# Kernel optimization log

Hardware: AMD Instinct MI355X
Metric: run time of the kernel (lower is better)

Reference implementation:

```python
import jax, jax.numpy as jnp
import numpy as np

B, T, C = 4, 2048, 1024
H = 16
D = C // H  # head_dim = 64

def setup_inputs() -> dict:
    key = jax.random.key(0)
    ks = jax.random.split(key, 5)
    s = 0.02
    return {
        "x": jax.random.normal(ks[0], (B, T, C), dtype=jnp.float32),
        "qkv_w": jax.random.normal(ks[1], (3 * C, C), dtype=jnp.float32) * s,
        "qkv_b": jax.random.normal(ks[2], (3 * C,), dtype=jnp.float32) * s,
        "proj_w": jax.random.normal(ks[3], (C, C), dtype=jnp.float32) * s,
        "proj_b": jax.random.normal(ks[4], (C,), dtype=jnp.float32) * s,
    }

def reference(x, qkv_w, qkv_b, proj_w, proj_b):
    Bx, Tx, Cx = x.shape
    # QKV projection (torch Linear: x @ W^T + b)
    qkv = x @ qkv_w.T + qkv_b                       # [B,T,3C]
    qkv = qkv.reshape(Bx, Tx, 3, H, D)
    qkv = jnp.transpose(qkv, (2, 0, 3, 1, 4))       # [3,B,H,T,D]
    q, k, v = qkv[0], qkv[1], qkv[2]
    scale = D ** -0.5
    attn = jnp.einsum("bhqd,bhkd->bhqk", q, k) * scale  # [B,H,T,T]
    causal = jnp.tril(jnp.ones((Tx, Tx), dtype=bool))
    attn = jnp.where(causal, attn, -jnp.inf)
    attn = jax.nn.softmax(attn, axis=-1)
    # dropout is identity in eval mode
    out = jnp.einsum("bhqk,bhkd->bhqd", attn, v)    # [B,H,T,D]
    out = jnp.transpose(out, (0, 2, 1, 3)).reshape(Bx, Tx, Cx)
    return out @ proj_w.T + proj_b
```

## Files before the change

### kernel.cpp

```cpp
#include <hip/hip_runtime.h>
#include <cstdint>
#include <cstddef>

#define B_ 4
#define T_ 2048
#define C_ 1024
#define H_ 16
#define D_ 64

typedef __bf16 bf16;
typedef __bf16 bf16x4 __attribute__((ext_vector_type(4)));
typedef __bf16 bf16x8 __attribute__((ext_vector_type(8)));
typedef float f32x4 __attribute__((ext_vector_type(4)));
typedef float f32x16 __attribute__((ext_vector_type(16)));
typedef unsigned int u32x4v __attribute__((ext_vector_type(4)));

typedef __attribute__((address_space(1))) void gvoid;
typedef __attribute__((address_space(3))) void lvoid;

__device__ __forceinline__ void async_load16(const void* g, void* l) {
    __builtin_amdgcn_global_load_lds((gvoid*)g, (lvoid*)l, 16, 0, 0);
}

__device__ __forceinline__ unsigned pk_bf16(float lo, float hi) {
    unsigned d;
    asm("v_cvt_pk_bf16_f32 %0, %1, %2" : "=v"(d) : "v"(lo), "v"(hi));
    return d;
}

__global__ __launch_bounds__(256) void fused_cast(
    const void* __restrict__ x, const void* __restrict__ wq,
    const void* __restrict__ bq, const void* __restrict__ wp,
    const void* __restrict__ bp,
    bf16* __restrict__ dx, bf16* __restrict__ dwq, bf16* __restrict__ dbq,
    bf16* __restrict__ dwp, bf16* __restrict__ dbp) {
    const int tid = threadIdx.x;
    __shared__ int cnt;
    if (tid == 0) cnt = 0;
    __syncthreads();
    const unsigned short* xu = (const unsigned short*)x;
    int local = 0;
#pragma unroll
    for (int j = 0; j < 16; ++j) {
        unsigned short u = xu[tid * 16 + j];
        if ((u & 0x7F80u) == 0x7F80u) local++;
    }
    atomicAdd(&cnt, local);
    __syncthreads();
    const bool f32in = cnt > 4;

    const int blk = blockIdx.x;
    const void* src;
    bf16* dst;
    int n, lb;
    if (blk < 4096)      { src = x;  dst = dx;  n = 8388608; lb = blk; }
    else if (blk < 5632) { src = wq; dst = dwq; n = 3145728; lb = blk - 4096; }
    else if (blk < 5634) { src = bq; dst = dbq; n = 3072;    lb = blk - 5632; }
    else if (blk < 6146) { src = wp; dst = dwp; n = 1048576; lb = blk - 5634; }
    else                 { src = bp; dst = dbp; n = 1024;    lb = 0; }

    const int i = lb * 2048 + tid * 8;
    if (i >= n) return;
    if (f32in) {
        const float* s = (const float*)src;
        bf16x8 v;
#pragma unroll
        for (int j = 0; j < 8; ++j) v[j] = (bf16)s[i + j];
        *(bf16x8*)&dst[i] = v;
    } else {
        *(bf16x8*)&dst[i] = *(const bf16x8*)((const bf16*)src + i);
    }
}

template <bool QKV>
__global__ __launch_bounds__(256) void gemm_bt(
    const bf16* __restrict__ A, const bf16* __restrict__ W,
    const bf16* __restrict__ bias, float* __restrict__ outf,
    bf16* __restrict__ q_ws, bf16* __restrict__ k_ws, bf16* __restrict__ vswz) {
    __shared__ bf16 As[2][128 * 64];
    __shared__ bf16 Bs[2][128 * 64];
    const int tid  = threadIdx.x;
    const int lane = tid & 63;
    const int wave = tid >> 6;
    const int lm = lane & 15;
    const int lg = lane >> 4;
    const int flat = blockIdx.y * gridDim.x + blockIdx.x;
    const int xcd = flat & 7;
    const int jsw = flat >> 3;
    const int bm0 = (xcd * 8 + (jsw & 7)) * 128;
    const int bn0 = (jsw >> 3) * 128;
    const int wm = (wave >> 1) * 64;
    const int wn = (wave & 1) * 64;

    f32x4 acc[4][4];
    const f32x4 z = {0.f, 0.f, 0.f, 0.f};
#pragma unroll
    for (int i = 0; i < 4; ++i)
#pragma unroll
        for (int j = 0; j < 4; ++j) acc[i][j] = z;

    const bf16* Ablk = A + (size_t)bm0 * 1024;
    const bf16* Wblk = W + (size_t)bn0 * 1024;

    auto stage = [&](int k0, int buf) {
#pragma unroll
        for (int j = 0; j < 4; ++j) {
            const int fb = (j << 8) + (wave << 6);
            const int f = fb + lane;
            const int row = f >> 3;
            const int col = ((f & 7) ^ (row & 7)) << 3;
            async_load16(Ablk + (size_t)row * 1024 + k0 + col, &As[buf][f * 8]);
            async_load16(Wblk + (size_t)row * 1024 + k0 + col, &Bs[buf][f * 8]);
        }
    };

    stage(0, 0);

    for (int kt = 0; kt < 16; ++kt) {
        const int cur = kt & 1;
        __syncthreads();

        if (kt + 1 < 16) stage((kt + 1) * 64, cur ^ 1);
        __builtin_amdgcn_sched_barrier(0);

#pragma unroll
        for (int ks = 0; ks < 2; ++ks) {
            bf16x8 af[4], bfr[4];
#pragma unroll
            for (int t = 0; t < 4; ++t) {
                const int ra = wm + t * 16 + lm;
                const int rb = wn + t * 16 + lm;
                const int c  = ks * 4 + lg;
                af[t]  = *(const bf16x8*)&As[cur][ra * 64 + ((c ^ (ra & 7)) << 3)];
                bfr[t] = *(const bf16x8*)&Bs[cur][rb * 64 + ((c ^ (rb & 7)) << 3)];
            }
#pragma unroll
            for (int mt = 0; mt < 4; ++mt)
#pragma unroll
                for (int nt = 0; nt < 4; ++nt)
                    acc[mt][nt] = __builtin_amdgcn_mfma_f32_16x16x32_bf16(
                        af[mt], bfr[nt], acc[mt][nt], 0, 0, 0);
        }
    }

#pragma unroll
    for (int mt = 0; mt < 4; ++mt) {
#pragma unroll
        for (int nt = 0; nt < 4; ++nt) {
            const int n = bn0 + wn + nt * 16 + lm;
            const float bn = (float)bias[n];
            const int mbase = bm0 + wm + mt * 16 + lg * 4;
            if (QKV) {
                const int part = n >> 10;
                const int h = (n >> 6) & 15;
                const int d = n & 63;
                const int b = mbase >> 11;
                const int t0 = mbase & 2047;
                if (part == 2) {
                    const int tl = t0 & 63;
                    const int kk = tl >> 4;
                    const int hv = (tl >> 3) & 1;
                    const int j0 = tl & 7;
                    const int dt = d >> 5;
                    const int dc = d & 31;
                    const int pos = ((dt * 4 + kk) * 64 + hv * 32 + dc) * 8 + j0;
                    bf16x4 pk;
#pragma unroll
                    for (int r = 0; r < 4; ++r)
                        pk[r] = (bf16)(acc[mt][nt][r] + bn);
                    *(bf16x4*)&vswz[((size_t)(b * 16 + h) * T_ + (t0 >> 6) * 64) * 64 +
                                    pos] = pk;
                } else {
                    bf16* dst = (part == 0) ? q_ws : k_ws;
#pragma unroll
                    for (int r = 0; r < 4; ++r)
                        dst[((size_t)((b * 16 + h) * 2048 + t0 + r) << 6) + d] =
                            (bf16)(acc[mt][nt][r] + bn);
                }
            } else {
#pragma unroll
                for (int r = 0; r < 4; ++r) {
                    const int m = mbase + r;
                    outf[(size_t)m * 1024 + n] = acc[mt][nt][r] + bn;
                }
            }
        }
    }
}

__global__ __launch_bounds__(256) void flash_attn(
    const bf16* __restrict__ q_ws, const bf16* __restrict__ k_ws,
    const bf16* __restrict__ vswz, bf16* __restrict__ att) {
    __shared__ bf16 Kf[2][4096];
    __shared__ bf16 Vf[2][4096];
    const int tid = threadIdx.x;
    const int lane = tid & 63;
    const int wave = tid >> 6;
    const int lq = lane & 31, hi = lane >> 5;
    const int flat = blockIdx.y * 64 + blockIdx.x;
    const int xcd = flat & 7;
    const int jsw = flat >> 3;
    const int bh = xcd * 8 + (jsw & 7);
    const int qt = 15 - (jsw >> 3);
    const int q0 = qt * 128;
    const int nkt = 2 * qt + 2;
    const bf16* Qb = q_ws + (size_t)bh * T_ * 64;
    const bf16* Kb = k_ws + (size_t)bh * T_ * 64;
    const bf16* Vz = vswz + (size_t)bh * T_ * 64;

    const int qrow = q0 + wave * 32 + lq;

    bf16x8 qf[4];
#pragma unroll
    for (int ds = 0; ds < 4; ++ds) {
        bf16x8 t = *(const bf16x8*)&Qb[(size_t)qrow * 64 + ds * 16 + hi * 8];
#pragma unroll
        for (int j = 0; j < 8; ++j) qf[ds][j] = (bf16)((float)t[j] * 0.18033688f);
    }

    bf16x8 onesf;
#pragma unroll
    for (int j = 0; j < 8; ++j) onesf[j] = (lq == 0) ? (bf16)1.0f : (bf16)0.0f;

    f32x16 of0, of1, lacc;
#pragma unroll
    for (int r = 0; r < 16; ++r) { of0[r] = 0.f; of1[r] = 0.f; lacc[r] = 0.f; }

#pragma unroll
    for (int jj = 0; jj < 2; ++jj) {
        const int c = wave * 2 + jj;
        const int kb = c >> 2, ds = c & 3;
        async_load16(Kb + (size_t)(kb * 32 + lq) * 64 + ds * 16 + hi * 8,
                     &Kf[0][(c * 64 + lane) * 8]);
        async_load16(Vz + (size_t)(c * 64 + lane) * 8, &Vf[0][(c * 64 + lane) * 8]);
    }

    for (int kt = 0; kt < nkt; ++kt) {
        const int cur = kt & 1;
        const int k0 = kt * 64;
        __syncthreads();

        if (kt + 1 < nkt) {
            const int k1 = k0 + 64;
#pragma unroll
            for (int jj = 0; jj < 2; ++jj) {
                const int c = wave * 2 + jj;
                const int kb = c >> 2, ds = c & 3;
                async_load16(Kb + (size_t)(k1 + kb * 32 + lq) * 64 + ds * 16 + hi * 8,
                             &Kf[cur ^ 1][(c * 64 + lane) * 8]);
                async_load16(Vz + (size_t)(kt + 1) * 4096 + (size_t)(c * 64 + lane) * 8,
                             &Vf[cur ^ 1][(c * 64 + lane) * 8]);
            }
        }

        bf16x8 pa[4];
#pragma unroll
        for (int kb = 0; kb < 2; ++kb) {
            f32x16 st;
#pragma unroll
            for (int r = 0; r < 16; ++r) st[r] = -28.85390082f;
            __builtin_amdgcn_s_setprio(1);
#pragma unroll
            for (int ds = 0; ds < 4; ++ds) {
                bf16x8 kf = *(const bf16x8*)&Kf[cur][((kb * 4 + ds) * 64 + lane) * 8];
                st = __builtin_amdgcn_mfma_f32_32x32x16_bf16(kf, qf[ds], st, 0, 0, 0);
            }
            __builtin_amdgcn_s_setprio(0);
            if (k0 + kb * 32 + 31 > q0 + wave * 32) {
#pragma unroll
                for (int r = 0; r < 16; ++r) {
                    const int kk_ = k0 + kb * 32 + (r & 3) + 8 * (r >> 2) + 4 * hi;
                    if (kk_ > qrow) st[r] = -1e30f;
                }
            }
            float p[16];
#pragma unroll
            for (int r = 0; r < 16; ++r)
                p[r] = __builtin_amdgcn_exp2f(st[r]);
            unsigned cg[4][2];
#pragma unroll
            for (int g = 0; g < 4; ++g) {
                cg[g][0] = pk_bf16(p[4 * g + 0], p[4 * g + 1]);
                cg[g][1] = pk_bf16(p[4 * g + 2], p[4 * g + 3]);
            }
#pragma unroll
            for (int m = 0; m < 2; ++m) {
                unsigned e0 = cg[2 * m][0], e1 = cg[2 * m][1];
                unsigned o0 = cg[2 * m + 1][0], o1 = cg[2 * m + 1][1];
                asm("v_permlane32_swap_b32 %0, %1" : "+v"(e0), "+v"(o0));
                asm("v_permlane32_swap_b32 %0, %1" : "+v"(e1), "+v"(o1));
                union { u32x4v u; bf16x8 h; } pk_;
                pk_.u = (u32x4v){e0, e1, o0, o1};
                pa[kb * 2 + m] = pk_.h;
            }
        }

        __builtin_amdgcn_s_setprio(1);
#pragma unroll
        for (int kk = 0; kk < 4; ++kk) {
            bf16x8 vf0 = *(const bf16x8*)&Vf[cur][((0 * 4 + kk) * 64 + lane) * 8];
            of0 = __builtin_amdgcn_mfma_f32_32x32x16_bf16(pa[kk], vf0, of0, 0, 0, 0);
            bf16x8 vf1 = *(const bf16x8*)&Vf[cur][((1 * 4 + kk) * 64 + lane) * 8];
            of1 = __builtin_amdgcn_mfma_f32_32x32x16_bf16(pa[kk], vf1, of1, 0, 0, 0);
            lacc = __builtin_amdgcn_mfma_f32_32x32x16_bf16(pa[kk], onesf, lacc, 0, 0, 0);
        }
        __builtin_amdgcn_s_setprio(0);
    }

    const int b = bh >> 4, h = bh & 15;
#pragma unroll
    for (int r = 0; r < 16; ++r) {
        const int cr = (r & 3) + 8 * (r >> 2) + 4 * hi;
        const int t = q0 + wave * 32 + cr;
        const float ls = __shfl(lacc[r], lane & 32);
        att[((size_t)(b * 2048 + t)) * 1024 + h * 64 + lq] = (bf16)(of0[r] / ls);
        att[((size_t)(b * 2048 + t)) * 1024 + h * 64 + 32 + lq] = (bf16)(of1[r] / ls);
    }
}

extern "C" void kernel_launch(void* const* d_in, const int* in_sizes, int n_in,
                              void* d_out, int out_size, void* d_ws, size_t ws_size,
                              hipStream_t stream) {
    float* out = (float*)d_out;

    const size_t SEG  = (size_t)B_ * H_ * T_ * D_;
    const size_t N_X  = (size_t)B_ * T_ * C_;
    const size_t N_WQ = (size_t)3 * C_ * C_;
    const size_t N_BQ = 3 * C_;
    const size_t N_WP = (size_t)C_ * C_;
    const size_t N_BP = C_;

    bf16* att   = (bf16*)d_ws;
    bf16* wqkv  = att + N_X;
    bf16* bqkv  = wqkv + N_WQ;
    bf16* wproj = bqkv + N_BQ;
    bf16* bproj = wproj + N_WP;
    bf16* qws   = bproj + N_BP;
    bf16* kws   = qws + SEG;
    bf16* vswz  = kws + SEG;
    bf16* xb    = (bf16*)d_out;

    fused_cast<<<6147, 256, 0, stream>>>(d_in[0], d_in[1], d_in[2], d_in[3],
                                         d_in[4], xb, wqkv, bqkv, wproj, bproj);

    gemm_bt<true><<<dim3(24, 64), 256, 0, stream>>>(xb, wqkv, bqkv, nullptr,
                                                    qws, kws, vswz);
    flash_attn<<<dim3(64, 16), 256, 0, stream>>>(qws, kws, vswz, att);
    gemm_bt<false><<<dim3(8, 64), 256, 0, stream>>>(att, wproj, bproj, out,
                                                    nullptr, nullptr, nullptr);
}
```

Baseline: 239.5 us.

## Process 64 query rows per wave in flash attention with 2-wave blocks

Each wave now handles two 32-row query sub-tiles instead of one, and the block shrinks from 4 to 2 waves while still covering 128 query rows. Each K/V fragment read from LDS is reused across two sets of MFMAs, halving LDS reads per unit of compute and giving more independent MFMA chains to interleave. The trade-off is roughly double the accumulator registers per wave and fewer waves per block, which can lower occupancy and latency hiding.

New measurement: 266.2 us. 1.11x slower.

```diff
diff --git a/kernel.cpp b/kernel.cpp
--- a/kernel.cpp
+++ b/kernel.cpp
@@ -188,7 +188,7 @@
     }
 }
 
-__global__ __launch_bounds__(256) void flash_attn(
+__global__ __launch_bounds__(128) void flash_attn(
     const bf16* __restrict__ q_ws, const bf16* __restrict__ k_ws,
     const bf16* __restrict__ vswz, bf16* __restrict__ att) {
     __shared__ bf16 Kf[2][4096];
@@ -208,27 +208,34 @@
     const bf16* Kb = k_ws + (size_t)bh * T_ * 64;
     const bf16* Vz = vswz + (size_t)bh * T_ * 64;
 
-    const int qrow = q0 + wave * 32 + lq;
-
-    bf16x8 qf[4];
-#pragma unroll
-    for (int ds = 0; ds < 4; ++ds) {
-        bf16x8 t = *(const bf16x8*)&Qb[(size_t)qrow * 64 + ds * 16 + hi * 8];
-#pragma unroll
-        for (int j = 0; j < 8; ++j) qf[ds][j] = (bf16)((float)t[j] * 0.18033688f);
-    }
+    const int qbase = q0 + wave * 64;
+
+    bf16x8 qf[2][4];
+#pragma unroll
+    for (int qh = 0; qh < 2; ++qh)
+#pragma unroll
+        for (int ds = 0; ds < 4; ++ds) {
+            bf16x8 t = *(const bf16x8*)&Qb[(size_t)(qbase + qh * 32 + lq) * 64 +
+                                           ds * 16 + hi * 8];
+#pragma unroll
+            for (int j = 0; j < 8; ++j) qf[qh][ds][j] = (bf16)((float)t[j] * 0.18033688f);
+        }
 
     bf16x8 onesf;
 #pragma unroll
     for (int j = 0; j < 8; ++j) onesf[j] = (lq == 0) ? (bf16)1.0f : (bf16)0.0f;
 
-    f32x16 of0, of1, lacc;
-#pragma unroll
-    for (int r = 0; r < 16; ++r) { of0[r] = 0.f; of1[r] = 0.f; lacc[r] = 0.f; }
-
-#pragma unroll
-    for (int jj = 0; jj < 2; ++jj) {
-        const int c = wave * 2 + jj;
+    f32x16 of[2][2], lacc[2];
+#pragma unroll
+    for (int r = 0; r < 16; ++r) {
+        of[0][0][r] = 0.f; of[0][1][r] = 0.f;
+        of[1][0][r] = 0.f; of[1][1][r] = 0.f;
+        lacc[0][r] = 0.f;  lacc[1][r] = 0.f;
+    }
+
+#pragma unroll
+    for (int jj = 0; jj < 4; ++jj) {
+        const int c = wave * 4 + jj;
         const int kb = c >> 2, ds = c & 3;
         async_load16(Kb + (size_t)(kb * 32 + lq) * 64 + ds * 16 + hi * 8,
                      &Kf[0][(c * 64 + lane) * 8]);
@@ -243,8 +250,8 @@
         if (kt + 1 < nkt) {
             const int k1 = k0 + 64;
 #pragma unroll
-            for (int jj = 0; jj < 2; ++jj) {
-                const int c = wave * 2 + jj;
+            for (int jj = 0; jj < 4; ++jj) {
+                const int c = wave * 4 + jj;
                 const int kb = c >> 2, ds = c & 3;
                 async_load16(Kb + (size_t)(k1 + kb * 32 + lq) * 64 + ds * 16 + hi * 8,
                              &Kf[cur ^ 1][(c * 64 + lane) * 8]);
@@ -253,45 +260,51 @@
             }
         }
 
-        bf16x8 pa[4];
+        bf16x8 pa[2][4];
 #pragma unroll
         for (int kb = 0; kb < 2; ++kb) {
-            f32x16 st;
-#pragma unroll
-            for (int r = 0; r < 16; ++r) st[r] = -28.85390082f;
+            f32x16 st0, st1;
+#pragma unroll
+            for (int r = 0; r < 16; ++r) { st0[r] = -28.85390082f; st1[r] = -28.85390082f; }
             __builtin_amdgcn_s_setprio(1);
 #pragma unroll
             for (int ds = 0; ds < 4; ++ds) {
                 bf16x8 kf = *(const bf16x8*)&Kf[cur][((kb * 4 + ds) * 64 + lane) * 8];
-                st = __builtin_amdgcn_mfma_f32_32x32x16_bf16(kf, qf[ds], st, 0, 0, 0);
+                st0 = __builtin_amdgcn_mfma_f32_32x32x16_bf16(kf, qf[0][ds], st0, 0, 0, 0);
+                st1 = __builtin_amdgcn_mfma_f32_32x32x16_bf16(kf, qf[1][ds], st1, 0, 0, 0);
             }
             __builtin_amdgcn_s_setprio(0);
-            if (k0 + kb * 32 + 31 > q0 + wave * 32) {
-#pragma unroll
-                for (int r = 0; r < 16; ++r) {
-                    const int kk_ = k0 + kb * 32 + (r & 3) + 8 * (r >> 2) + 4 * hi;
-                    if (kk_ > qrow) st[r] = -1e30f;
-                }
-            }
-            float p[16];
-#pragma unroll
-            for (int r = 0; r < 16; ++r)
-                p[r] = __builtin_amdgcn_exp2f(st[r]);
-            unsigned cg[4][2];
-#pragma unroll
-            for (int g = 0; g < 4; ++g) {
-                cg[g][0] = pk_bf16(p[4 * g + 0], p[4 * g + 1]);
-                cg[g][1] = pk_bf16(p[4 * g + 2], p[4 * g + 3]);
-            }
-#pragma unroll
-            for (int m = 0; m < 2; ++m) {
-                unsigned e0 = cg[2 * m][0], e1 = cg[2 * m][1];
-                unsigned o0 = cg[2 * m + 1][0], o1 = cg[2 * m + 1][1];
-                asm("v_permlane32_swap_b32 %0, %1" : "+v"(e0), "+v"(o0));
-                asm("v_permlane32_swap_b32 %0, %1" : "+v"(e1), "+v"(o1));
-                union { u32x4v u; bf16x8 h; } pk_;
-                pk_.u = (u32x4v){e0, e1, o0, o1};
-                pa[kb * 2 + m] = pk_.h;
+#pragma unroll
+            for (int qh = 0; qh < 2; ++qh) {
+                f32x16 st = qh ? st1 : st0;
+                const int qminw = qbase + qh * 32;
+                if (k0 + kb * 32 + 31 > qminw) {
+#pragma unroll
+                    for (int r = 0; r < 16; ++r) {
+                        const int kk_ = k0 + kb * 32 + (r & 3) + 8 * (r >> 2) + 4 * hi;
+                        if (kk_ > qminw + lq) st[r] = -1e30f;
+                    }
+                }
+                float p[16];
+#pragma unroll
+                for (int r = 0; r < 16; ++r)
+                    p[r] = __builtin_amdgcn_exp2f(st[r]);
+                unsigned cg[4][2];
+#pragma unroll
+                for (int g = 0; g < 4; ++g) {
+                    cg[g][0] = pk_bf16(p[4 * g + 0], p[4 * g + 1]);
+                    cg[g][1] = pk_bf16(p[4 * g + 2], p[4 * g + 3]);
+                }
+#pragma unroll
+                for (int m = 0; m < 2; ++m) {
+                    unsigned e0 = cg[2 * m][0], e1 = cg[2 * m][1];
+                    unsigned o0 = cg[2 * m + 1][0], o1 = cg[2 * m + 1][1];
+                    asm("v_permlane32_swap_b32 %0, %1" : "+v"(e0), "+v"(o0));
+                    asm("v_permlane32_swap_b32 %0, %1" : "+v"(e1), "+v"(o1));
+                    union { u32x4v u; bf16x8 h; } pk_;
+                    pk_.u = (u32x4v){e0, e1, o0, o1};
+                    pa[qh][kb * 2 + m] = pk_.h;
+                }
             }
         }
 
@@ -299,22 +312,28 @@
 #pragma unroll
         for (int kk = 0; kk < 4; ++kk) {
             bf16x8 vf0 = *(const bf16x8*)&Vf[cur][((0 * 4 + kk) * 64 + lane) * 8];
-            of0 = __builtin_amdgcn_mfma_f32_32x32x16_bf16(pa[kk], vf0, of0, 0, 0, 0);
+            of[0][0] = __builtin_amdgcn_mfma_f32_32x32x16_bf16(pa[0][kk], vf0, of[0][0], 0, 0, 0);
+            of[1][0] = __builtin_amdgcn_mfma_f32_32x32x16_bf16(pa[1][kk], vf0, of[1][0], 0, 0, 0);
             bf16x8 vf1 = *(const bf16x8*)&Vf[cur][((1 * 4 + kk) * 64 + lane) * 8];
-            of1 = __builtin_amdgcn_mfma_f32_32x32x16_bf16(pa[kk], vf1, of1, 0, 0, 0);
-            lacc = __builtin_amdgcn_mfma_f32_32x32x16_bf16(pa[kk], onesf, lacc, 0, 0, 0);
+            of[0][1] = __builtin_amdgcn_mfma_f32_32x32x16_bf16(pa[0][kk], vf1, of[0][1], 0, 0, 0);
+            of[1][1] = __builtin_amdgcn_mfma_f32_32x32x16_bf16(pa[1][kk], vf1, of[1][1], 0, 0, 0);
+            lacc[0] = __builtin_amdgcn_mfma_f32_32x32x16_bf16(pa[0][kk], onesf, lacc[0], 0, 0, 0);
+            lacc[1] = __builtin_amdgcn_mfma_f32_32x32x16_bf16(pa[1][kk], onesf, lacc[1], 0, 0, 0);
         }
         __builtin_amdgcn_s_setprio(0);
     }
 
     const int b = bh >> 4, h = bh & 15;
 #pragma unroll
-    for (int r = 0; r < 16; ++r) {
-        const int cr = (r & 3) + 8 * (r >> 2) + 4 * hi;
-        const int t = q0 + wave * 32 + cr;
-        const float ls = __shfl(lacc[r], lane & 32);
-        att[((size_t)(b * 2048 + t)) * 1024 + h * 64 + lq] = (bf16)(of0[r] / ls);
-        att[((size_t)(b * 2048 + t)) * 1024 + h * 64 + 32 + lq] = (bf16)(of1[r] / ls);
+    for (int qh = 0; qh < 2; ++qh) {
+#pragma unroll
+        for (int r = 0; r < 16; ++r) {
+            const int cr = (r & 3) + 8 * (r >> 2) + 4 * hi;
+            const int t = qbase + qh * 32 + cr;
+            const float ls = __shfl(lacc[qh][r], lane & 32);
+            att[((size_t)(b * 2048 + t)) * 1024 + h * 64 + lq] = (bf16)(of[qh][0][r] / ls);
+            att[((size_t)(b * 2048 + t)) * 1024 + h * 64 + 32 + lq] = (bf16)(of[qh][1][r] / ls);
+        }
     }
 }
 
@@ -345,7 +364,7 @@
 
     gemm_bt<true><<<dim3(24, 64), 256, 0, stream>>>(xb, wqkv, bqkv, nullptr,
                                                     qws, kws, vswz);
-    flash_attn<<<dim3(64, 16), 256, 0, stream>>>(qws, kws, vswz, att);
+    flash_attn<<<dim3(64, 16), 128, 0, stream>>>(qws, kws, vswz, att);
     gemm_bt<false><<<dim3(8, 64), 256, 0, stream>>>(att, wproj, bproj, out,
                                                     nullptr, nullptr, nullptr);
 }
```
